# Kernel tuning notes

Hardware: AMD Instinct MI355X
Metric: run time of the kernel (lower is better)

The kernel has to match this reference:

```python
import jax, jax.numpy as jnp
import numpy as np

SCALE = 0.5
DROP_P = 0.2

def setup_inputs() -> dict:
    key = jax.random.key(0)
    k1, k2 = jax.random.split(key)
    x1 = jax.random.normal(k1, (8, 2048, 128), dtype=jnp.float32)
    x2 = jax.random.normal(k2, (8, 2048, 128), dtype=jnp.float32)
    return {"x1": x1, "x2": x2}

def reference(x1, x2):
    # scores: [B, M, N] = x1 @ x2^T, scaled by 0.5
    scores = jnp.einsum('bmd,bnd->bmn', x1, x2) * SCALE
    probs = jax.nn.softmax(scores, axis=-1)
    # dropout p=0.2 (training mode in the torch source); fixed key for determinism
    keep = jax.random.bernoulli(jax.random.key(42), 1.0 - DROP_P, probs.shape)
    probs = jnp.where(keep, probs / (1.0 - DROP_P), 0.0)
    # out: [B, M, D] = probs @ x2
    return jnp.einsum('bmn,bnd->bmd', probs, x2)
```

## Files before the change

kernel.cpp:

```cpp
#include <hip/hip_runtime.h>
#include <stdint.h>


typedef __bf16 bf16x8 __attribute__((ext_vector_type(8)));
typedef float f32x4 __attribute__((ext_vector_type(4)));

union FragAB {
  bf16x8 v;
  uint32_t u[4];
};

__device__ __forceinline__ uint32_t rotl32(uint32_t x, uint32_t r) {
  return (x << r) | (x >> (32u - r));
}

__device__ __forceinline__ void threefry2x32_k42(uint32_t in0, uint32_t in1,
                                                 uint32_t& o0, uint32_t& o1) {
  const uint32_t ks0 = 0u;
  const uint32_t ks1 = 42u;
  const uint32_t ks2 = 0x1BD11BDAu ^ 0u ^ 42u;
  uint32_t x0 = in0 + ks0;
  uint32_t x1 = in1 + ks1;
#define TFR(r) { x0 += x1; x1 = rotl32(x1, r); x1 ^= x0; }
  TFR(13u) TFR(15u) TFR(26u) TFR(6u)
  x0 += ks1; x1 += ks2 + 1u;
  TFR(17u) TFR(29u) TFR(16u) TFR(24u)
  x0 += ks2; x1 += ks0 + 2u;
  TFR(13u) TFR(15u) TFR(26u) TFR(6u)
  x0 += ks0; x1 += ks1 + 3u;
  TFR(17u) TFR(29u) TFR(16u) TFR(24u)
  x0 += ks1; x1 += ks2 + 4u;
  TFR(13u) TFR(15u) TFR(26u) TFR(6u)
  x0 += ks2; x1 += ks0 + 5u;
#undef TFR
  o0 = x0; o1 = x1;
}

__device__ __forceinline__ uint32_t pack_bf16(float a, float b) {
  __bf16 ba = (__bf16)a;
  __bf16 bb = (__bf16)b;
  uint32_t ua = (uint32_t)__builtin_bit_cast(uint16_t, ba);
  uint32_t ub = (uint32_t)__builtin_bit_cast(uint16_t, bb);
  return ua | (ub << 16);
}

#define KEEP_LT 3435974144u
#define MBIAS 40.0f

__launch_bounds__(256, 2)
__global__ void attn_kernel(const float* __restrict__ x1,
                            const float* __restrict__ x2,
                            float* __restrict__ out) {
  __shared__ __attribute__((aligned(16))) uint32_t SMEM[4][4800];

  const int tid = threadIdx.x;
  const int wv = __builtin_amdgcn_readfirstlane(tid >> 6);
  const int lane = tid & 63;
  const int l15 = lane & 15;
  const int g = lane >> 4;
  const int b = blockIdx.y;
  const int m0 = blockIdx.x * 32;

  uint32_t* KtW = &SMEM[wv][0];
  uint32_t* VtW = &SMEM[wv][2176];
  uint32_t* PbW = &SMEM[wv][4480];

  const float QSCALE = 0.5f * 1.44269504088896340736f;
  FragAB qf[2][4];
  #pragma unroll
  for (int s = 0; s < 2; ++s) {
    const float* qp_base = x1 + ((size_t)b * 2048 + m0 + s * 16 + l15) * 128;
    #pragma unroll
    for (int c = 0; c < 4; ++c) {
      const float* qp = qp_base + c * 32 + g * 8;
      float4 f0 = *(const float4*)(qp);
      float4 f1 = *(const float4*)(qp + 4);
      qf[s][c].u[0] = pack_bf16(f0.x * QSCALE, f0.y * QSCALE);
      qf[s][c].u[1] = pack_bf16(f0.z * QSCALE, f0.w * QSCALE);
      qf[s][c].u[2] = pack_bf16(f1.x * QSCALE, f1.y * QSCALE);
      qf[s][c].u[3] = pack_bf16(f1.z * QSCALE, f1.w * QSCALE);
    }
  }

  f32x4 o[2][8];
  #pragma unroll
  for (int s = 0; s < 2; ++s)
    #pragma unroll
    for (int dt = 0; dt < 8; ++dt) o[s][dt] = (f32x4){0.f, 0.f, 0.f, 0.f};
  float lsum[2] = {0.f, 0.f};

  uint32_t rb[2];
  #pragma unroll
  for (int s = 0; s < 2; ++s)
    rb[s] = (uint32_t)b * 4194304u +
            (uint32_t)(m0 + s * 16 + l15) * 2048u + (uint32_t)(wv * 512);

  const float4* x2b4 = (const float4*)(x2 + (size_t)b * 2048 * 128);
  const uint32_t permsel = (l15 & 1) ? 0x07060302u : 0x05040100u;

  for (int tile = 0; tile < 16; ++tile) {
    const int n0g = wv * 512 + tile * 32;

    #pragma unroll
    for (int i = 0; i < 16; ++i) {
      int n = 2 * i + (lane >> 5);
      int dq = lane & 31;
      float4 v = x2b4[(size_t)(n0g + n) * 32 + dq];
      uint32_t p0 = pack_bf16(v.x, v.y);
      uint32_t p1 = pack_bf16(v.z, v.w);
      *(uint2*)&KtW[n * 68 + 2 * dq] = make_uint2(p0, p1);
      VtW[dq * 36 + n] = p0;
      VtW[(dq + 32) * 36 + n] = p1;
    }
    asm volatile("s_waitcnt lgkmcnt(0)" ::: "memory");

    f32x4 sa[2][2];
    #pragma unroll
    for (int s = 0; s < 2; ++s)
      #pragma unroll
      for (int t = 0; t < 2; ++t) sa[s][t] = (f32x4){0.f, 0.f, 0.f, 0.f};
    #pragma unroll
    for (int c = 0; c < 4; ++c) {
      FragAB k0, k1;
      uint4 a0 = *(const uint4*)&KtW[l15 * 68 + c * 16 + 4 * g];
      uint4 a1 = *(const uint4*)&KtW[(16 + l15) * 68 + c * 16 + 4 * g];
      k0.u[0] = a0.x; k0.u[1] = a0.y; k0.u[2] = a0.z; k0.u[3] = a0.w;
      k1.u[0] = a1.x; k1.u[1] = a1.y; k1.u[2] = a1.z; k1.u[3] = a1.w;
      sa[0][0] = __builtin_amdgcn_mfma_f32_16x16x32_bf16(k0.v, qf[0][c].v, sa[0][0], 0, 0, 0);
      sa[0][1] = __builtin_amdgcn_mfma_f32_16x16x32_bf16(k1.v, qf[0][c].v, sa[0][1], 0, 0, 0);
      sa[1][0] = __builtin_amdgcn_mfma_f32_16x16x32_bf16(k0.v, qf[1][c].v, sa[1][0], 0, 0, 0);
      sa[1][1] = __builtin_amdgcn_mfma_f32_16x16x32_bf16(k1.v, qf[1][c].v, sa[1][1], 0, 0, 0);
    }

    FragAB pa[2];
    #pragma unroll
    for (int s = 0; s < 2; ++s) {
      #pragma unroll
      for (int t = 0; t < 2; ++t) {
        float p0 = __builtin_amdgcn_exp2f(sa[s][t][0] - MBIAS);
        float p1 = __builtin_amdgcn_exp2f(sa[s][t][1] - MBIAS);
        float p2 = __builtin_amdgcn_exp2f(sa[s][t][2] - MBIAS);
        float p3 = __builtin_amdgcn_exp2f(sa[s][t][3] - MBIAS);
        lsum[s] += (p0 + p1) + (p2 + p3);
        uint32_t ib = rb[s] + (uint32_t)(tile * 32 + t * 16 + 4 * g);
        uint32_t h0, h1, bits;
        threefry2x32_k42(0u, ib + 0u, h0, h1); bits = h0 ^ h1;
        float q0 = (bits < KEEP_LT) ? p0 : 0.0f;
        threefry2x32_k42(0u, ib + 1u, h0, h1); bits = h0 ^ h1;
        float q1 = (bits < KEEP_LT) ? p1 : 0.0f;
        threefry2x32_k42(0u, ib + 2u, h0, h1); bits = h0 ^ h1;
        float q2 = (bits < KEEP_LT) ? p2 : 0.0f;
        threefry2x32_k42(0u, ib + 3u, h0, h1); bits = h0 ^ h1;
        float q3 = (bits < KEEP_LT) ? p3 : 0.0f;
        *(uint2*)&PbW[l15 * 20 + t * 8 + 2 * g] =
            make_uint2(pack_bf16(q0, q1), pack_bf16(q2, q3));
      }
      asm volatile("s_waitcnt lgkmcnt(0)" ::: "memory");
      uint4 pu = *(const uint4*)&PbW[l15 * 20 + 4 * g];
      pa[s].u[0] = pu.x; pa[s].u[1] = pu.y; pa[s].u[2] = pu.z; pa[s].u[3] = pu.w;
    }

    #pragma unroll
    for (int dt = 0; dt < 8; ++dt) {
      int rowp = ((l15 >> 1) & 1) * 32 + 4 * dt + (l15 >> 2);
      const uint32_t* vr = &VtW[rowp * 36 + 8 * g];
      uint4 U0 = *(const uint4*)vr;
      uint4 U1 = *(const uint4*)(vr + 4);
      FragAB vb;
      vb.u[0] = __builtin_amdgcn_perm(U0.y, U0.x, permsel);
      vb.u[1] = __builtin_amdgcn_perm(U0.w, U0.z, permsel);
      vb.u[2] = __builtin_amdgcn_perm(U1.y, U1.x, permsel);
      vb.u[3] = __builtin_amdgcn_perm(U1.w, U1.z, permsel);
      o[0][dt] = __builtin_amdgcn_mfma_f32_16x16x32_bf16(pa[0].v, vb.v, o[0][dt], 0, 0, 0);
      o[1][dt] = __builtin_amdgcn_mfma_f32_16x16x32_bf16(pa[1].v, vb.v, o[1][dt], 0, 0, 0);
    }
  }

  __syncthreads();
  float* EP = (float*)&SMEM[0][0];
  #pragma unroll
  for (int s = 0; s < 2; ++s) {
    #pragma unroll
    for (int dt = 0; dt < 8; ++dt)
      #pragma unroll
      for (int r = 0; r < 4; ++r)
        EP[(((wv * 2 + s) * 8 + dt) * 4 + r) * 64 + lane] = o[s][dt][r];
    EP[16384 + (s * 16 + l15) * 16 + wv * 4 + g] = lsum[s];
  }
  __syncthreads();
  const int s = wv >> 1;
  float scale[4];
  #pragma unroll
  for (int r = 0; r < 4; ++r) {
    const float4* lp = (const float4*)&EP[16384 + (s * 16 + 4 * g + r) * 16];
    float4 A = lp[0], B4 = lp[1], C4 = lp[2], D4 = lp[3];
    float L = ((A.x + A.y) + (A.z + A.w)) + ((B4.x + B4.y) + (B4.z + B4.w)) +
              ((C4.x + C4.y) + (C4.z + C4.w)) + ((D4.x + D4.y) + (D4.z + D4.w));
    scale[r] = 1.0f / (L * 0.8f);
  }
  #pragma unroll
  for (int it = 0; it < 4; ++it) {
    int dt = (wv * 4 + it) & 7;
    #pragma unroll
    for (int r = 0; r < 4; ++r) {
      int base = ((s * 8 + dt) * 4 + r) * 64 + lane;
      float tot = EP[base] + EP[base + 4096] + EP[base + 8192] + EP[base + 12288];
      out[((size_t)b * 2048 + m0 + s * 16 + 4 * g + r) * 128 + dt * 16 + l15] =
          tot * scale[r];
    }
  }
}

extern "C" void kernel_launch(void* const* d_in, const int* in_sizes, int n_in,
                              void* d_out, int out_size, void* d_ws, size_t ws_size,
                              hipStream_t stream) {
  const float* x1 = (const float*)d_in[0];
  const float* x2 = (const float*)d_in[1];
  float* out = (float*)d_out;
  dim3 grid(64, 8, 1);
  dim3 block(256, 1, 1);
  attn_kernel<<<grid, block, 0, stream>>>(x1, x2, out);
}
```

Baseline: 155.6 us.

## Prepack K/V into MFMA fragment layout in workspace, stream fragments from global

Adds a prep kernel that converts x2 to bf16 once and writes it into MFMA-ready K and V fragment layouts in the workspace. The attention kernel then loads those fragments straight from global or L2 instead of converting and transposing x2 through LDS in every block. Each block now handles 16 query rows instead of 32, which doubles the grid and raises the occupancy target. The cost is an extra kernel launch plus a workspace round trip, and each K/V fragment is now read by twice as many blocks. The old path stays as a fallback when no workspace is available.

Result: faster. 146.1 us (-6.1%).

```diff
diff --git a/kernel.cpp b/kernel.cpp
--- a/kernel.cpp
+++ b/kernel.cpp
@@ -46,6 +46,176 @@
 
 #define KEEP_LT 3435974144u
 #define MBIAS 40.0f
+
+__launch_bounds__(256, 4)
+__global__ void prep_kernel(const float* __restrict__ x2,
+                            uint4* __restrict__ KF,
+                            uint4* __restrict__ VF) {
+  const int tid = threadIdx.x;
+  const int w = tid >> 6;
+  const int lane = tid & 63;
+  const int l15 = lane & 15;
+  const int g = lane >> 4;
+  const int T = blockIdx.x;
+  const int b = blockIdx.y;
+  const float* xb = x2 + (size_t)b * 2048 * 128;
+
+  #pragma unroll
+  for (int h = 0; h < 2; ++h) {
+    const int n = T * 32 + h * 16 + l15;
+    const float* p = xb + (size_t)n * 128 + w * 32 + 8 * g;
+    float4 f0 = *(const float4*)(p);
+    float4 f1 = *(const float4*)(p + 4);
+    uint4 u;
+    u.x = pack_bf16(f0.x, f0.y);
+    u.y = pack_bf16(f0.z, f0.w);
+    u.z = pack_bf16(f1.x, f1.y);
+    u.w = pack_bf16(f1.z, f1.w);
+    KF[(size_t)((b * 64 + T) * 8 + w * 2 + h) * 64 + lane] = u;
+  }
+
+  #pragma unroll
+  for (int i = 0; i < 2; ++i) {
+    const int dt = w + 4 * i;
+    const int d = dt * 16 + l15;
+    const float* p = xb + (size_t)(T * 32 + 8 * g) * 128 + d;
+    uint4 u;
+    u.x = pack_bf16(p[0],   p[128]);
+    u.y = pack_bf16(p[256], p[384]);
+    u.z = pack_bf16(p[512], p[640]);
+    u.w = pack_bf16(p[768], p[896]);
+    VF[(size_t)((b * 64 + T) * 8 + dt) * 64 + lane] = u;
+  }
+}
+
+__launch_bounds__(256, 4)
+__global__ void attn2_kernel(const float* __restrict__ x1,
+                             const uint4* __restrict__ KF,
+                             const uint4* __restrict__ VF,
+                             float* __restrict__ out) {
+  __shared__ __attribute__((aligned(16))) uint32_t SMEM[8768];
+
+  const int tid = threadIdx.x;
+  const int w = __builtin_amdgcn_readfirstlane(tid >> 6);
+  const int lane = tid & 63;
+  const int l15 = lane & 15;
+  const int g = lane >> 4;
+  const int b = blockIdx.y;
+  const int m0 = blockIdx.x * 16;
+
+  uint32_t* PbW = &SMEM[w * 320];
+
+  const float QSCALE = 0.5f * 1.44269504088896340736f;
+  FragAB qf[4];
+  {
+    const float* qp_base = x1 + ((size_t)b * 2048 + m0 + l15) * 128;
+    #pragma unroll
+    for (int c = 0; c < 4; ++c) {
+      const float* qp = qp_base + c * 32 + g * 8;
+      float4 f0 = *(const float4*)(qp);
+      float4 f1 = *(const float4*)(qp + 4);
+      qf[c].u[0] = pack_bf16(f0.x * QSCALE, f0.y * QSCALE);
+      qf[c].u[1] = pack_bf16(f0.z * QSCALE, f0.w * QSCALE);
+      qf[c].u[2] = pack_bf16(f1.x * QSCALE, f1.y * QSCALE);
+      qf[c].u[3] = pack_bf16(f1.z * QSCALE, f1.w * QSCALE);
+    }
+  }
+
+  f32x4 o[8];
+  #pragma unroll
+  for (int dt = 0; dt < 8; ++dt) o[dt] = (f32x4){0.f, 0.f, 0.f, 0.f};
+  float lsum = 0.f;
+
+  const uint32_t rb = (uint32_t)b * 4194304u +
+                      (uint32_t)(m0 + l15) * 2048u + (uint32_t)(w * 512);
+
+  const uint4* kfp = KF + (size_t)((b * 64 + w * 16) * 8) * 64 + lane;
+  const uint4* vfp = VF + (size_t)((b * 64 + w * 16) * 8) * 64 + lane;
+
+  for (int tile = 0; tile < 16; ++tile) {
+    f32x4 sa[2];
+    sa[0] = (f32x4){0.f, 0.f, 0.f, 0.f};
+    sa[1] = (f32x4){0.f, 0.f, 0.f, 0.f};
+    #pragma unroll
+    for (int c = 0; c < 4; ++c) {
+      uint4 a0 = kfp[(c * 2 + 0) * 64];
+      uint4 a1 = kfp[(c * 2 + 1) * 64];
+      FragAB k0, k1;
+      k0.u[0] = a0.x; k0.u[1] = a0.y; k0.u[2] = a0.z; k0.u[3] = a0.w;
+      k1.u[0] = a1.x; k1.u[1] = a1.y; k1.u[2] = a1.z; k1.u[3] = a1.w;
+      sa[0] = __builtin_amdgcn_mfma_f32_16x16x32_bf16(k0.v, qf[c].v, sa[0], 0, 0, 0);
+      sa[1] = __builtin_amdgcn_mfma_f32_16x16x32_bf16(k1.v, qf[c].v, sa[1], 0, 0, 0);
+    }
+
+    #pragma unroll
+    for (int t = 0; t < 2; ++t) {
+      float p0 = __builtin_amdgcn_exp2f(sa[t][0] - MBIAS);
+      float p1 = __builtin_amdgcn_exp2f(sa[t][1] - MBIAS);
+      float p2 = __builtin_amdgcn_exp2f(sa[t][2] - MBIAS);
+      float p3 = __builtin_amdgcn_exp2f(sa[t][3] - MBIAS);
+      lsum += (p0 + p1) + (p2 + p3);
+      uint32_t ib = rb + (uint32_t)(tile * 32 + t * 16 + 4 * g);
+      uint32_t h0, h1, bits;
+      threefry2x32_k42(0u, ib + 0u, h0, h1); bits = h0 ^ h1;
+      float q0 = (bits < KEEP_LT) ? p0 : 0.0f;
+      threefry2x32_k42(0u, ib + 1u, h0, h1); bits = h0 ^ h1;
+      float q1 = (bits < KEEP_LT) ? p1 : 0.0f;
+      threefry2x32_k42(0u, ib + 2u, h0, h1); bits = h0 ^ h1;
+      float q2 = (bits < KEEP_LT) ? p2 : 0.0f;
+      threefry2x32_k42(0u, ib + 3u, h0, h1); bits = h0 ^ h1;
+      float q3 = (bits < KEEP_LT) ? p3 : 0.0f;
+      *(uint2*)&PbW[l15 * 20 + t * 8 + 2 * g] =
+          make_uint2(pack_bf16(q0, q1), pack_bf16(q2, q3));
+    }
+    asm volatile("s_waitcnt lgkmcnt(0)" ::: "memory");
+    FragAB pa;
+    {
+      uint4 pu = *(const uint4*)&PbW[l15 * 20 + 4 * g];
+      pa.u[0] = pu.x; pa.u[1] = pu.y; pa.u[2] = pu.z; pa.u[3] = pu.w;
+    }
+
+    #pragma unroll
+    for (int dt = 0; dt < 8; ++dt) {
+      uint4 vv = vfp[dt * 64];
+      FragAB vb;
+      vb.u[0] = vv.x; vb.u[1] = vv.y; vb.u[2] = vv.z; vb.u[3] = vv.w;
+      o[dt] = __builtin_amdgcn_mfma_f32_16x16x32_bf16(pa.v, vb.v, o[dt], 0, 0, 0);
+    }
+    kfp += 512;
+    vfp += 512;
+  }
+
+  __syncthreads();
+  float* EP = (float*)&SMEM[0];
+  float* EPL = EP + 8192;
+  EPL[l15 * 36 + w * 4 + g] = lsum;
+  #pragma unroll
+  for (int dt = 0; dt < 8; ++dt)
+    #pragma unroll
+    for (int r = 0; r < 4; ++r)
+      EP[((w * 8 + dt) * 4 + r) * 64 + lane] = o[dt][r];
+  __syncthreads();
+  float scale[4];
+  #pragma unroll
+  for (int r = 0; r < 4; ++r) {
+    const float4* lp = (const float4*)&EPL[(4 * g + r) * 36];
+    float4 A = lp[0], B4 = lp[1], C4 = lp[2], D4 = lp[3];
+    float L = ((A.x + A.y) + (A.z + A.w)) + ((B4.x + B4.y) + (B4.z + B4.w)) +
+              ((C4.x + C4.y) + (C4.z + C4.w)) + ((D4.x + D4.y) + (D4.z + D4.w));
+    scale[r] = 1.0f / (L * 0.8f);
+  }
+  #pragma unroll
+  for (int i = 0; i < 2; ++i) {
+    const int dt = w * 2 + i;
+    #pragma unroll
+    for (int r = 0; r < 4; ++r) {
+      int base = (dt * 4 + r) * 64 + lane;
+      float tot = EP[base] + EP[base + 2048] + EP[base + 4096] + EP[base + 6144];
+      out[((size_t)b * 2048 + m0 + 4 * g + r) * 128 + dt * 16 + l15] =
+          tot * scale[r];
+    }
+  }
+}
 
 __launch_bounds__(256, 2)
 __global__ void attn_kernel(const float* __restrict__ x1,
@@ -217,7 +387,12 @@
   const float* x1 = (const float*)d_in[0];
   const float* x2 = (const float*)d_in[1];
   float* out = (float*)d_out;
-  dim3 grid(64, 8, 1);
-  dim3 block(256, 1, 1);
-  attn_kernel<<<grid, block, 0, stream>>>(x1, x2, out);
-}
+  if (d_ws != nullptr && ws_size >= (size_t)8 * 1024 * 1024) {
+    uint4* KF = (uint4*)d_ws;
+    uint4* VF = KF + 262144;
+    prep_kernel<<<dim3(64, 8, 1), dim3(256, 1, 1), 0, stream>>>(x2, KF, VF);
+    attn2_kernel<<<dim3(128, 8, 1), dim3(256, 1, 1), 0, stream>>>(x1, KF, VF, out);
+  } else {
+    attn_kernel<<<dim3(64, 8, 1), dim3(256, 1, 1), 0, stream>>>(x1, x2, out);
+  }
+}
```
